# Kernel tuning notes

Measured on AMD Instinct MI355X. Metric: run time of the kernel, lower is better.

## Reference

```python
import jax, jax.numpy as jnp
import numpy as np

B, LQ, LK, D, H = 2, 1024, 1024, 1024, 16
DH = D // H


def setup_inputs() -> dict:
    key = jax.random.key(0)
    ks = jax.random.split(key, 14)
    s = 1.0 / np.sqrt(D)
    inp = {
        "q": jax.random.normal(ks[0], (B, LQ, D), jnp.float32),
        "k": jax.random.normal(ks[1], (B, LK, D), jnp.float32),
        "v": jax.random.normal(ks[2], (B, LK, D), jnp.float32),
        "Wq": jax.random.normal(ks[3], (D, D), jnp.float32) * s,
        "bq": jnp.zeros((D,), jnp.float32),
        "Wk": jax.random.normal(ks[4], (D, D), jnp.float32) * s,
        "bk": jnp.zeros((D,), jnp.float32),
        "Wv": jax.random.normal(ks[5], (D, D), jnp.float32) * s,
        "bv": jnp.zeros((D,), jnp.float32),
        "Wo": jax.random.normal(ks[6], (D, D), jnp.float32) * s,
        "bo": jnp.zeros((D,), jnp.float32),
        "logits_bias": jax.random.normal(ks[7], (B, LQ, LK), jnp.float32),
        "key_padding_mask": jax.random.randint(ks[8], (B, LK), 0, 2) > 0,
    }
    return inp


def _split_heads(x):
    b, l, _ = x.shape
    return x.reshape(b, l, H, DH).transpose(0, 2, 1, 3)  # [B,H,L,DH]


def reference(q, k, v, Wq, bq, Wk, bk, Wv, bv, Wo, bo, logits_bias, key_padding_mask):
    qh = _split_heads(q @ Wq.T + bq)  # [B,H,Lq,DH]
    kh = _split_heads(k @ Wk.T + bk)  # [B,H,Lk,DH]
    vh = _split_heads(v @ Wv.T + bv)  # [B,H,Lk,DH]

    neg = jnp.finfo(qh.dtype).min
    # attn_mask = logits_bias broadcast over heads, masked_fill at padded keys
    attn_mask = jnp.where(key_padding_mask[:, None, None, :],
                          neg, logits_bias[:, None, :, :])  # [B,1,Lq,Lk]

    scale = 1.0 / np.sqrt(DH)
    scores = jnp.einsum('bhqd,bhkd->bhqk', qh, kh) * scale + attn_mask
    probs = jax.nn.softmax(scores, axis=-1)
    out = jnp.einsum('bhqk,bhkd->bhqd', probs, vh)  # [B,H,Lq,DH]
    out = out.transpose(0, 2, 1, 3).reshape(q.shape[0], q.shape[1], D)
    return out @ Wo.T + bo
```

## Files before the change

kernel.cpp:

```cpp
#include <hip/hip_runtime.h>


typedef _Float16 half8 __attribute__((ext_vector_type(8)));
typedef _Float16 half4_t __attribute__((ext_vector_type(4)));
typedef float f32x4 __attribute__((ext_vector_type(4)));

#define MFMA16(a, b, c) __builtin_amdgcn_mfma_f32_16x16x32_f16((a), (b), (c), 0, 0, 0)

#define WAITCNT_VM(n) asm volatile("s_waitcnt vmcnt(" #n ")" ::: "memory")
#define WAITCNT_LGKM0() asm volatile("s_waitcnt lgkmcnt(0)" ::: "memory")
#define RAW_BARRIER() asm volatile("s_barrier" ::: "memory")
#define EXP2F(x) __builtin_amdgcn_exp2f(x)

__device__ __forceinline__ void gload16(const void* g, void* l) {
  __builtin_amdgcn_global_load_lds(
      (const __attribute__((address_space(1))) unsigned int*)g,
      (__attribute__((address_space(3))) unsigned int*)l, 16, 0, 0);
}

__device__ __forceinline__ half8 frag_ld(const _Float16* t, int row, int ck) {
  return *(const half8*)(t + row * 64 + (((ck ^ (row & 7)) << 3)));
}

__global__ __launch_bounds__(256) void cvt_f32_f16(
    const float* __restrict__ q, const float* __restrict__ k, const float* __restrict__ v,
    const float* __restrict__ Wq, const float* __restrict__ Wk,
    const float* __restrict__ Wv, const float* __restrict__ Wo,
    _Float16* __restrict__ q16, _Float16* __restrict__ k16, _Float16* __restrict__ v16,
    _Float16* __restrict__ w16) {
  const int y = blockIdx.y;
  if (y >= 3 && blockIdx.x >= 512) return;
  const float* s;
  _Float16* d;
  const size_t M = (size_t)1024 * 1024;
  switch (y) {
    case 0: s = q;  d = q16; break;
    case 1: s = k;  d = k16; break;
    case 2: s = v;  d = v16; break;
    case 3: s = Wq; d = w16; break;
    case 4: s = Wk; d = w16 + M; break;
    case 5: s = Wv; d = w16 + 2 * M; break;
    default: s = Wo; d = w16 + 3 * M; break;
  }
  const size_t i = ((size_t)blockIdx.x * 256 + threadIdx.x) * 8;
  const float4 a = *(const float4*)(s + i);
  const float4 bvv = *(const float4*)(s + i + 4);
  half8 h;
  h[0] = (_Float16)a.x; h[1] = (_Float16)a.y; h[2] = (_Float16)a.z; h[3] = (_Float16)a.w;
  h[4] = (_Float16)bvv.x; h[5] = (_Float16)bvv.y; h[6] = (_Float16)bvv.z; h[7] = (_Float16)bvv.w;
  *(half8*)(d + i) = h;
}

__global__ __launch_bounds__(256) void cvt_bias(
    const float* __restrict__ biasL, const int* __restrict__ kpm,
    _Float16* __restrict__ biasC) {
  const size_t i = ((size_t)blockIdx.x * 256 + threadIdx.x) * 8;
  const int b = (int)(i >> 20);
  const int kk = (int)(i & 1023);
  const int* mrow = kpm + (b << 10) + kk;
  const float4 b0 = *(const float4*)(biasL + i);
  const float4 b1 = *(const float4*)(biasL + i + 4);
  const int4 m0 = *(const int4*)mrow;
  const int4 m1 = *(const int4*)(mrow + 4);
  const float sc = 1.44269504f;
  half8 h;
  h[0] = m0.x ? (_Float16)-30000.f : (_Float16)(b0.x * sc);
  h[1] = m0.y ? (_Float16)-30000.f : (_Float16)(b0.y * sc);
  h[2] = m0.z ? (_Float16)-30000.f : (_Float16)(b0.z * sc);
  h[3] = m0.w ? (_Float16)-30000.f : (_Float16)(b0.w * sc);
  h[4] = m1.x ? (_Float16)-30000.f : (_Float16)(b1.x * sc);
  h[5] = m1.y ? (_Float16)-30000.f : (_Float16)(b1.y * sc);
  h[6] = m1.z ? (_Float16)-30000.f : (_Float16)(b1.z * sc);
  h[7] = m1.w ? (_Float16)-30000.f : (_Float16)(b1.w * sc);
  *(half8*)(biasC + i) = h;
}

__global__ __launch_bounds__(256) void mmp(
    const _Float16* __restrict__ Aq, const _Float16* __restrict__ Ak,
    const _Float16* __restrict__ Av, const _Float16* __restrict__ W16,
    const float* __restrict__ c0, const float* __restrict__ c1,
    const float* __restrict__ c2, _Float16* __restrict__ Dq,
    _Float16* __restrict__ Dk, _Float16* __restrict__ Dvt,
    float* __restrict__ Df, int is_final) {
  __shared__ __align__(16) _Float16 lds[24576];

  const int tid = threadIdx.x;
  const int wv = tid >> 6, ln = tid & 63;
  const int quad = ln >> 4, col = ln & 15;
  const int wm = wv >> 1, wn = wv & 1;
  const int n0 = blockIdx.x * 128;
  const int m0 = blockIdx.y * 64;
  const int z = blockIdx.z;

  const _Float16* A = (z == 0) ? Aq : (z == 1) ? Ak : Av;
  const _Float16* Bw = W16 + (size_t)z * 1024 * 1024;
  const float* bias = (z == 0) ? c0 : (z == 1) ? c1 : c2;

  auto stage = [&](int buf, int k0) {
#pragma unroll
    for (int j = 0; j < 6; ++j) {
      const int ci = j * 256 + tid;
      const _Float16* src;
      if (ci < 512) {
        const int row = ci >> 3, lc = (ci & 7) ^ (row & 7);
        src = A + (size_t)(m0 + row) * 1024 + k0 + lc * 8;
      } else {
        const int di = ci - 512;
        const int row = di >> 3, lc = (di & 7) ^ (row & 7);
        src = Bw + (size_t)(n0 + row) * 1024 + k0 + lc * 8;
      }
      gload16(src, lds + buf * 12288 + (j * 256 + wv * 64) * 8);
    }
  };

  const f32x4 zero4 = {0.f, 0.f, 0.f, 0.f};
  f32x4 acc[2][4];
#pragma unroll
  for (int i = 0; i < 2; ++i)
#pragma unroll
    for (int j = 0; j < 4; ++j) acc[i][j] = zero4;

  stage(0, 0);
  for (int i = 0; i < 15; ++i) {
    stage((i + 1) & 1, (i + 1) * 64);
    WAITCNT_VM(6);
    RAW_BARRIER();
    const _Float16* As = lds + (i & 1) * 12288;
    const _Float16* Bs = As + 4096;
    half8 af[2][2], bf[2][4];
#pragma unroll
    for (int kk = 0; kk < 2; ++kk) {
#pragma unroll
      for (int mi = 0; mi < 2; ++mi)
        af[kk][mi] = frag_ld(As, wm * 32 + mi * 16 + col, kk * 4 + quad);
#pragma unroll
      for (int ni = 0; ni < 4; ++ni)
        bf[kk][ni] = frag_ld(Bs, wn * 64 + ni * 16 + col, kk * 4 + quad);
    }
    WAITCNT_LGKM0();
    RAW_BARRIER();
#pragma unroll
    for (int kk = 0; kk < 2; ++kk)
#pragma unroll
      for (int mi = 0; mi < 2; ++mi)
#pragma unroll
        for (int ni = 0; ni < 4; ++ni)
          acc[mi][ni] = MFMA16(af[kk][mi], bf[kk][ni], acc[mi][ni]);
  }
  {
    WAITCNT_VM(0);
    RAW_BARRIER();
    const _Float16* As = lds + 12288;
    const _Float16* Bs = As + 4096;
#pragma unroll
    for (int kk = 0; kk < 2; ++kk) {
      half8 af[2], bf[4];
#pragma unroll
      for (int mi = 0; mi < 2; ++mi)
        af[mi] = frag_ld(As, wm * 32 + mi * 16 + col, kk * 4 + quad);
#pragma unroll
      for (int ni = 0; ni < 4; ++ni)
        bf[ni] = frag_ld(Bs, wn * 64 + ni * 16 + col, kk * 4 + quad);
#pragma unroll
      for (int mi = 0; mi < 2; ++mi)
#pragma unroll
        for (int ni = 0; ni < 4; ++ni)
          acc[mi][ni] = MFMA16(af[mi], bf[ni], acc[mi][ni]);
    }
  }

  float bv[4];
#pragma unroll
  for (int ni = 0; ni < 4; ++ni) bv[ni] = bias[n0 + wn * 64 + ni * 16 + col];

  if (is_final) {
#pragma unroll
    for (int mi = 0; mi < 2; ++mi) {
      const int m_g = m0 + wm * 32 + mi * 16 + quad * 4;
#pragma unroll
      for (int ni = 0; ni < 4; ++ni) {
        const int n_g = n0 + wn * 64 + ni * 16 + col;
#pragma unroll
        for (int r = 0; r < 4; ++r)
          Df[(size_t)(m_g + r) * 1024 + n_g] = acc[mi][ni][r] + bv[ni];
      }
    }
  } else if (z < 2) {
    _Float16* D = z ? Dk : Dq;
#pragma unroll
    for (int mi = 0; mi < 2; ++mi) {
      const int m_g = m0 + wm * 32 + mi * 16 + quad * 4;
#pragma unroll
      for (int ni = 0; ni < 4; ++ni) {
        const int n_g = n0 + wn * 64 + ni * 16 + col;
        const int h = n_g >> 6, dh = n_g & 63;
#pragma unroll
        for (int r = 0; r < 4; ++r) {
          const int b = (m_g + r) >> 10, l = (m_g + r) & 1023;
          D[((size_t)((b * 16 + h) * 1024) + l) * 64 + dh] =
              (_Float16)(acc[mi][ni][r] + bv[ni]);
        }
      }
    }
  } else {
    __syncthreads();
    _Float16* Ct = lds;
#pragma unroll
    for (int mi = 0; mi < 2; ++mi) {
      const int ml = wm * 32 + mi * 16 + quad * 4;
#pragma unroll
      for (int ni = 0; ni < 4; ++ni) {
        const int nl = wn * 64 + ni * 16 + col;
#pragma unroll
        for (int r = 0; r < 4; ++r)
          Ct[(size_t)nl * 72 + ml + r] = (_Float16)(acc[mi][ni][r] + bv[ni]);
      }
    }
    __syncthreads();
#pragma unroll
    for (int it = 0; it < 4; ++it) {
      const int ci = it * 256 + tid;
      const int n = ci >> 3;
      const int mc = (ci & 7) * 8;
      const half8 hv = *(const half8*)(Ct + (size_t)n * 72 + mc);
      const int n_g = n0 + n;
      const int h = n_g >> 6, dh = n_g & 63;
      const int m_g = m0 + mc;
      const int b = m_g >> 10, l = m_g & 1023;
      *(half8*)(Dvt + ((size_t)((b * 16 + h) * 64 + dh)) * 1024 + l) = hv;
    }
  }
}

__global__ __launch_bounds__(512, 4) void attn(
    const _Float16* __restrict__ Qh, const _Float16* __restrict__ Kh,
    const _Float16* __restrict__ Vt, const _Float16* __restrict__ biasC,
    _Float16* __restrict__ AO) {
  __shared__ __align__(16) _Float16 KV[2 * 8192];
  __shared__ __align__(16) _Float16 Pt[8][512];

  const int tid = threadIdx.x;
  const int wv = tid >> 6, ln = tid & 63;
  const int quad = ln >> 4, col = ln & 15;
  const int qsub = wv >> 1, khalf = wv & 1;
  const int q0 = blockIdx.x * 64;
  const int bh = blockIdx.y;
  const int b = bh >> 4, hh = bh & 15;
  const int qg = q0 + qsub * 16 + col;

  const _Float16* Qp = Qh + ((size_t)bh * 1024 + qg) * 64;
  const half8 bq0 = *(const half8*)(Qp + quad * 8);
  const half8 bq1 = *(const half8*)(Qp + 32 + quad * 8);
  WAITCNT_VM(0);

  const _Float16* biasRow = biasC + ((size_t)(b * 1024 + qg)) * 1024;

  auto stageKV = [&](int buf, int it) {
    const int koff = it * 64;
#pragma unroll
    for (int j = 0; j < 2; ++j) {
      const int ci = j * 512 + tid;
      const void* src;
      if (ci < 512) {
        const int row = ci >> 3, lc = (ci & 7) ^ (row & 7);
        src = Kh + ((size_t)bh * 1024 + koff + row) * 64 + lc * 8;
      } else {
        const int di = ci - 512;
        const int row = di >> 3, lc = (di & 7) ^ (row & 7);
        src = Vt + ((size_t)bh * 64 + row) * 1024 + koff + lc * 8;
      }
      gload16(src, KV + buf * 8192 + (j * 512 + wv * 64) * 8);
    }
  };
  auto loadBias = [&](int it, half4_t* bb) {
    const int koff = it * 64 + khalf * 32;
#pragma unroll
    for (int mi = 0; mi < 2; ++mi)
      bb[mi] = *(const half4_t*)&biasRow[koff + mi * 16 + quad * 4];
  };

  const f32x4 zero4 = {0.f, 0.f, 0.f, 0.f};
  f32x4 o[4];
#pragma unroll
  for (int ni = 0; ni < 4; ++ni) o[ni] = zero4;
  float m_i = -1e30f, l_i = 0.f;
  _Float16* Pw = Pt[wv];

  auto compute = [&](int buf, const half4_t* bb) {
    const _Float16* Ks = KV + buf * 8192;
    const _Float16* Vs = Ks + 4096;
    f32x4 s[2];
#pragma unroll
    for (int mi = 0; mi < 2; ++mi) {
      f32x4 a4 = zero4;
      a4 = MFMA16(frag_ld(Ks, khalf * 32 + mi * 16 + col, quad), bq0, a4);
      a4 = MFMA16(frag_ld(Ks, khalf * 32 + mi * 16 + col, 4 + quad), bq1, a4);
      s[mi] = a4;
    }
#pragma unroll
    for (int mi = 0; mi < 2; ++mi)
#pragma unroll
      for (int r = 0; r < 4; ++r)
        s[mi][r] = s[mi][r] * 0.18033688f + (float)bb[mi][r];
    float rm = fmaxf(fmaxf(fmaxf(s[0][0], s[0][1]), fmaxf(s[0][2], s[0][3])),
                     fmaxf(fmaxf(s[1][0], s[1][1]), fmaxf(s[1][2], s[1][3])));
    rm = fmaxf(rm, __shfl_xor(rm, 16));
    rm = fmaxf(rm, __shfl_xor(rm, 32));
    const float mn = fmaxf(m_i, rm);
    const float alpha = EXP2F(m_i - mn);
    m_i = mn;
    float ps = 0.f;
#pragma unroll
    for (int mi = 0; mi < 2; ++mi)
#pragma unroll
      for (int r = 0; r < 4; ++r) {
        const float p = EXP2F(s[mi][r] - mn);
        s[mi][r] = p;
        ps += p;
      }
    ps += __shfl_xor(ps, 16);
    ps += __shfl_xor(ps, 32);
    l_i = l_i * alpha + ps;
#pragma unroll
    for (int ni = 0; ni < 4; ++ni)
#pragma unroll
      for (int r = 0; r < 4; ++r) o[ni][r] *= alpha;
#pragma unroll
    for (int mi = 0; mi < 2; ++mi) {
      half4_t h;
      h[0] = (_Float16)s[mi][0]; h[1] = (_Float16)s[mi][1];
      h[2] = (_Float16)s[mi][2]; h[3] = (_Float16)s[mi][3];
      const int kloc = mi * 16 + quad * 4;
      *(half4_t*)(Pw + col * 32 + ((((kloc >> 3) ^ (col & 3)) << 3) | (kloc & 7))) = h;
    }
    const half8 p0 = *(const half8*)(Pw + col * 32 + ((quad ^ (col & 3)) << 3));
#pragma unroll
    for (int ni = 0; ni < 4; ++ni)
      o[ni] = MFMA16(frag_ld(Vs, ni * 16 + col, khalf * 4 + quad), p0, o[ni]);
  };

  half4_t bbA[2], bbB[2];
  stageKV(0, 0);
  loadBias(0, bbA);
  for (int i = 0; i < 15; ++i) {
    stageKV((i + 1) & 1, i + 1);
    loadBias(i + 1, bbB);
    WAITCNT_VM(4);
    RAW_BARRIER();
    compute(i & 1, bbA);
    WAITCNT_LGKM0();
    RAW_BARRIER();
    bbA[0] = bbB[0]; bbA[1] = bbB[1];
  }
  WAITCNT_VM(0);
  RAW_BARRIER();
  compute(1, bbA);

  __syncthreads();
  f32x4* Ox = (f32x4*)&KV[0];
  float* MlS = (float*)&KV[8192];
  if (khalf == 1) {
#pragma unroll
    for (int ni = 0; ni < 4; ++ni) Ox[(qsub * 4 + ni) * 64 + ln] = o[ni];
    MlS[qsub * 64 + ln] = m_i;
    MlS[256 + qsub * 64 + ln] = l_i;
  }
  __syncthreads();
  if (khalf == 0) {
    const float m2 = MlS[qsub * 64 + ln];
    const float l2 = MlS[256 + qsub * 64 + ln];
    const float ms = fmaxf(m_i, m2);
    const float w1 = EXP2F(m_i - ms);
    const float w2 = EXP2F(m2 - ms);
    const float inv = 1.0f / (l_i * w1 + l2 * w2);
#pragma unroll
    for (int ni = 0; ni < 4; ++ni) {
      const f32x4 o2 = Ox[(qsub * 4 + ni) * 64 + ln];
      half4_t h;
#pragma unroll
      for (int r = 0; r < 4; ++r)
        h[r] = (_Float16)((o[ni][r] * w1 + o2[r] * w2) * inv);
      *(half4_t*)&AO[((size_t)(b * 1024 + qg)) * 1024 + hh * 64 + ni * 16 + quad * 4] = h;
    }
  }
}

extern "C" void kernel_launch(void* const* d_in, const int* in_sizes, int n_in,
                              void* d_out, int out_size, void* d_ws, size_t ws_size,
                              hipStream_t stream) {
  (void)in_sizes; (void)n_in; (void)out_size; (void)ws_size;
  const float* q = (const float*)d_in[0];
  const float* k = (const float*)d_in[1];
  const float* v = (const float*)d_in[2];
  const float* Wq = (const float*)d_in[3];
  const float* bq = (const float*)d_in[4];
  const float* Wk = (const float*)d_in[5];
  const float* bk = (const float*)d_in[6];
  const float* Wv = (const float*)d_in[7];
  const float* bv = (const float*)d_in[8];
  const float* Wo = (const float*)d_in[9];
  const float* bo = (const float*)d_in[10];
  const float* lb = (const float*)d_in[11];
  const int* kpm = (const int*)d_in[12];
  float* out = (float*)d_out;

  const size_t NT = (size_t)2 * 1024 * 1024;
  _Float16* q16 = (_Float16*)d_ws;
  _Float16* k16 = q16 + NT;
  _Float16* v16 = k16 + NT;
  _Float16* Qh = v16 + NT;
  _Float16* Kh = Qh + NT;
  _Float16* Vt = Kh + NT;
  _Float16* w16 = Vt + NT;
  _Float16* AO = q16;
  _Float16* biasC = k16;

  cvt_f32_f16<<<dim3(1024, 7), 256, 0, stream>>>(q, k, v, Wq, Wk, Wv, Wo,
                                                 q16, k16, v16, w16);
  mmp<<<dim3(8, 32, 3), 256, 0, stream>>>(q16, k16, v16, w16, bq, bk, bv,
                                          Qh, Kh, Vt, nullptr, 0);
  cvt_bias<<<dim3(1024), 256, 0, stream>>>(lb, kpm, biasC);
  attn<<<dim3(16, 32), 512, 0, stream>>>(Qh, Kh, Vt, biasC, AO);
  mmp<<<dim3(8, 32, 1), 256, 0, stream>>>(AO, nullptr, nullptr, w16 + 3 * NT / 2,
                                          bo, nullptr, nullptr, nullptr, nullptr,
                                          nullptr, out, 1);
}
```

Baseline: 174.1 us.

## Fold bias conversion into cvt kernel and use 128x128 tiles for QKV projection

The separate cvt_bias launch is merged into cvt_f32_f16 as an extra grid row, and the bias buffer moves to its own workspace region so it no longer aliases k16, which the QKV projection now reads concurrently. The QKV projection switches to a new mmp_big kernel with 128x128 output tiles, 4x4 MFMA accumulators per wave and 64-wide double-buffered K stages, which raises data reuse per tile. This removes one launch and halves the grid of the projection in exchange for higher register and LDS use per block, which may lower occupancy.

```diff
diff --git a/kernel.cpp b/kernel.cpp
--- a/kernel.cpp
+++ b/kernel.cpp
@@ -26,9 +26,32 @@
     const float* __restrict__ q, const float* __restrict__ k, const float* __restrict__ v,
     const float* __restrict__ Wq, const float* __restrict__ Wk,
     const float* __restrict__ Wv, const float* __restrict__ Wo,
+    const float* __restrict__ biasL, const int* __restrict__ kpm,
     _Float16* __restrict__ q16, _Float16* __restrict__ k16, _Float16* __restrict__ v16,
-    _Float16* __restrict__ w16) {
+    _Float16* __restrict__ w16, _Float16* __restrict__ biasC) {
   const int y = blockIdx.y;
+  if (y == 7) {
+    const size_t i = ((size_t)blockIdx.x * 256 + threadIdx.x) * 8;
+    const int b = (int)(i >> 20);
+    const int kk = (int)(i & 1023);
+    const int* mrow = kpm + (b << 10) + kk;
+    const float4 b0 = *(const float4*)(biasL + i);
+    const float4 b1 = *(const float4*)(biasL + i + 4);
+    const int4 m0 = *(const int4*)mrow;
+    const int4 m1 = *(const int4*)(mrow + 4);
+    const float sc = 1.44269504f;
+    half8 h;
+    h[0] = m0.x ? (_Float16)-30000.f : (_Float16)(b0.x * sc);
+    h[1] = m0.y ? (_Float16)-30000.f : (_Float16)(b0.y * sc);
+    h[2] = m0.z ? (_Float16)-30000.f : (_Float16)(b0.z * sc);
+    h[3] = m0.w ? (_Float16)-30000.f : (_Float16)(b0.w * sc);
+    h[4] = m1.x ? (_Float16)-30000.f : (_Float16)(b1.x * sc);
+    h[5] = m1.y ? (_Float16)-30000.f : (_Float16)(b1.y * sc);
+    h[6] = m1.z ? (_Float16)-30000.f : (_Float16)(b1.z * sc);
+    h[7] = m1.w ? (_Float16)-30000.f : (_Float16)(b1.w * sc);
+    *(half8*)(biasC + i) = h;
+    return;
+  }
   if (y >= 3 && blockIdx.x >= 512) return;
   const float* s;
   _Float16* d;
@@ -51,28 +74,155 @@
   *(half8*)(d + i) = h;
 }
 
-__global__ __launch_bounds__(256) void cvt_bias(
-    const float* __restrict__ biasL, const int* __restrict__ kpm,
-    _Float16* __restrict__ biasC) {
-  const size_t i = ((size_t)blockIdx.x * 256 + threadIdx.x) * 8;
-  const int b = (int)(i >> 20);
-  const int kk = (int)(i & 1023);
-  const int* mrow = kpm + (b << 10) + kk;
-  const float4 b0 = *(const float4*)(biasL + i);
-  const float4 b1 = *(const float4*)(biasL + i + 4);
-  const int4 m0 = *(const int4*)mrow;
-  const int4 m1 = *(const int4*)(mrow + 4);
-  const float sc = 1.44269504f;
-  half8 h;
-  h[0] = m0.x ? (_Float16)-30000.f : (_Float16)(b0.x * sc);
-  h[1] = m0.y ? (_Float16)-30000.f : (_Float16)(b0.y * sc);
-  h[2] = m0.z ? (_Float16)-30000.f : (_Float16)(b0.z * sc);
-  h[3] = m0.w ? (_Float16)-30000.f : (_Float16)(b0.w * sc);
-  h[4] = m1.x ? (_Float16)-30000.f : (_Float16)(b1.x * sc);
-  h[5] = m1.y ? (_Float16)-30000.f : (_Float16)(b1.y * sc);
-  h[6] = m1.z ? (_Float16)-30000.f : (_Float16)(b1.z * sc);
-  h[7] = m1.w ? (_Float16)-30000.f : (_Float16)(b1.w * sc);
-  *(half8*)(biasC + i) = h;
+__global__ __launch_bounds__(256, 2) void mmp_big(
+    const _Float16* __restrict__ Aq, const _Float16* __restrict__ Ak,
+    const _Float16* __restrict__ Av, const _Float16* __restrict__ W16,
+    const float* __restrict__ c0, const float* __restrict__ c1,
+    const float* __restrict__ c2, _Float16* __restrict__ Dq,
+    _Float16* __restrict__ Dk, _Float16* __restrict__ Dvt) {
+  __shared__ __align__(16) _Float16 lds[32768];
+
+  const int tid = threadIdx.x;
+  const int wv = tid >> 6, ln = tid & 63;
+  const int quad = ln >> 4, col = ln & 15;
+  const int wm = wv >> 1, wn = wv & 1;
+  const int n0 = blockIdx.x * 128;
+  const int m0 = blockIdx.y * 128;
+  const int z = blockIdx.z;
+
+  const _Float16* A = (z == 0) ? Aq : (z == 1) ? Ak : Av;
+  const _Float16* Bw = W16 + (size_t)z * 1024 * 1024;
+  const float* bias = (z == 0) ? c0 : (z == 1) ? c1 : c2;
+
+  auto stage = [&](int buf, int k0) {
+#pragma unroll
+    for (int j = 0; j < 8; ++j) {
+      const int ci = j * 256 + tid;
+      const _Float16* src;
+      if (ci < 1024) {
+        const int row = ci >> 3, lc = (ci & 7) ^ (row & 7);
+        src = A + (size_t)(m0 + row) * 1024 + k0 + lc * 8;
+      } else {
+        const int di = ci - 1024;
+        const int row = di >> 3, lc = (di & 7) ^ (row & 7);
+        src = Bw + (size_t)(n0 + row) * 1024 + k0 + lc * 8;
+      }
+      gload16(src, lds + buf * 16384 + (j * 256 + wv * 64) * 8);
+    }
+  };
+
+  const f32x4 zero4 = {0.f, 0.f, 0.f, 0.f};
+  f32x4 acc[4][4];
+#pragma unroll
+  for (int i = 0; i < 4; ++i)
+#pragma unroll
+    for (int j = 0; j < 4; ++j) acc[i][j] = zero4;
+
+  stage(0, 0);
+  for (int i = 0; i < 15; ++i) {
+    stage((i + 1) & 1, (i + 1) * 64);
+    WAITCNT_VM(8);
+    RAW_BARRIER();
+    const _Float16* As = lds + (i & 1) * 16384;
+    const _Float16* Bs = As + 8192;
+    half8 af0[4], bf0[4], af1[4], bf1[4];
+#pragma unroll
+    for (int mi = 0; mi < 4; ++mi) af0[mi] = frag_ld(As, wm * 64 + mi * 16 + col, quad);
+#pragma unroll
+    for (int ni = 0; ni < 4; ++ni) bf0[ni] = frag_ld(Bs, wn * 64 + ni * 16 + col, quad);
+#pragma unroll
+    for (int mi = 0; mi < 4; ++mi) af1[mi] = frag_ld(As, wm * 64 + mi * 16 + col, 4 + quad);
+#pragma unroll
+    for (int ni = 0; ni < 4; ++ni) bf1[ni] = frag_ld(Bs, wn * 64 + ni * 16 + col, 4 + quad);
+    WAITCNT_LGKM0();
+    RAW_BARRIER();
+#pragma unroll
+    for (int mi = 0; mi < 4; ++mi)
+#pragma unroll
+      for (int ni = 0; ni < 4; ++ni)
+        acc[mi][ni] = MFMA16(af0[mi], bf0[ni], acc[mi][ni]);
+#pragma unroll
+    for (int mi = 0; mi < 4; ++mi)
+#pragma unroll
+      for (int ni = 0; ni < 4; ++ni)
+        acc[mi][ni] = MFMA16(af1[mi], bf1[ni], acc[mi][ni]);
+  }
+  {
+    WAITCNT_VM(0);
+    RAW_BARRIER();
+    const _Float16* As = lds + 16384;
+    const _Float16* Bs = As + 8192;
+    half8 af0[4], bf0[4], af1[4], bf1[4];
+#pragma unroll
+    for (int mi = 0; mi < 4; ++mi) af0[mi] = frag_ld(As, wm * 64 + mi * 16 + col, quad);
+#pragma unroll
+    for (int ni = 0; ni < 4; ++ni) bf0[ni] = frag_ld(Bs, wn * 64 + ni * 16 + col, quad);
+#pragma unroll
+    for (int mi = 0; mi < 4; ++mi) af1[mi] = frag_ld(As, wm * 64 + mi * 16 + col, 4 + quad);
+#pragma unroll
+    for (int ni = 0; ni < 4; ++ni) bf1[ni] = frag_ld(Bs, wn * 64 + ni * 16 + col, 4 + quad);
+#pragma unroll
+    for (int mi = 0; mi < 4; ++mi)
+#pragma unroll
+      for (int ni = 0; ni < 4; ++ni)
+        acc[mi][ni] = MFMA16(af0[mi], bf0[ni], acc[mi][ni]);
+#pragma unroll
+    for (int mi = 0; mi < 4; ++mi)
+#pragma unroll
+      for (int ni = 0; ni < 4; ++ni)
+        acc[mi][ni] = MFMA16(af1[mi], bf1[ni], acc[mi][ni]);
+  }
+
+  float bv[4];
+#pragma unroll
+  for (int ni = 0; ni < 4; ++ni) bv[ni] = bias[n0 + wn * 64 + ni * 16 + col];
+
+  if (z < 2) {
+    _Float16* D = z ? Dk : Dq;
+#pragma unroll
+    for (int mi = 0; mi < 4; ++mi) {
+      const int m_g = m0 + wm * 64 + mi * 16 + quad * 4;
+#pragma unroll
+      for (int ni = 0; ni < 4; ++ni) {
+        const int n_g = n0 + wn * 64 + ni * 16 + col;
+        const int h = n_g >> 6, dh = n_g & 63;
+#pragma unroll
+        for (int r = 0; r < 4; ++r) {
+          const int b = (m_g + r) >> 10, l = (m_g + r) & 1023;
+          D[((size_t)((b * 16 + h) * 1024) + l) * 64 + dh] =
+              (_Float16)(acc[mi][ni][r] + bv[ni]);
+        }
+      }
+    }
+  } else {
+    __syncthreads();
+    _Float16* Ct = lds;
+#pragma unroll
+    for (int mi = 0; mi < 4; ++mi) {
+      const int ml = wm * 64 + mi * 16 + quad * 4;
+#pragma unroll
+      for (int ni = 0; ni < 4; ++ni) {
+        const int nl = wn * 64 + ni * 16 + col;
+        half4_t h;
+#pragma unroll
+        for (int r = 0; r < 4; ++r) h[r] = (_Float16)(acc[mi][ni][r] + bv[ni]);
+        *(half4_t*)(Ct + (size_t)nl * 136 + ml) = h;
+      }
+    }
+    __syncthreads();
+#pragma unroll
+    for (int it = 0; it < 8; ++it) {
+      const int ci = it * 256 + tid;
+      const int n = ci >> 4;
+      const int mc = (ci & 15) * 8;
+      const half8 hv = *(const half8*)(Ct + (size_t)n * 136 + mc);
+      const int n_g = n0 + n;
+      const int h = n_g >> 6, dh = n_g & 63;
+      const int m_g = m0 + mc;
+      const int b = m_g >> 10, l = m_g & 1023;
+      *(half8*)(Dvt + ((size_t)((b * 16 + h) * 64 + dh)) * 1024 + l) = hv;
+    }
+  }
 }
 
 __global__ __launch_bounds__(256) void mmp(
@@ -412,14 +562,13 @@
   _Float16* Kh = Qh + NT;
   _Float16* Vt = Kh + NT;
   _Float16* w16 = Vt + NT;
+  _Float16* biasC = w16 + 4 * (NT / 2);
   _Float16* AO = q16;
-  _Float16* biasC = k16;
-
-  cvt_f32_f16<<<dim3(1024, 7), 256, 0, stream>>>(q, k, v, Wq, Wk, Wv, Wo,
-                                                 q16, k16, v16, w16);
-  mmp<<<dim3(8, 32, 3), 256, 0, stream>>>(q16, k16, v16, w16, bq, bk, bv,
-                                          Qh, Kh, Vt, nullptr, 0);
-  cvt_bias<<<dim3(1024), 256, 0, stream>>>(lb, kpm, biasC);
+
+  cvt_f32_f16<<<dim3(1024, 8), 256, 0, stream>>>(q, k, v, Wq, Wk, Wv, Wo, lb, kpm,
+                                                 q16, k16, v16, w16, biasC);
+  mmp_big<<<dim3(8, 16, 3), 256, 0, stream>>>(q16, k16, v16, w16, bq, bk, bv,
+                                              Qh, Kh, Vt);
   attn<<<dim3(16, 32), 512, 0, stream>>>(Qh, Kh, Vt, biasC, AO);
   mmp<<<dim3(8, 32, 1), 256, 0, stream>>>(AO, nullptr, nullptr, w16 + 3 * NT / 2,
                                           bo, nullptr, nullptr, nullptr, nullptr,
```

After: 170.1 us. -2.3%, faster.
